# Performance work log

Measured on AMD Instinct MI355X. Metric: run time of the kernel, lower is better.

## Reference

```python
import jax, jax.numpy as jnp
import numpy as np

N_WIRES = 16
DIM = 2 ** N_WIRES
BSZ = 512
FFN_DIM = 64
N_BLOCKS = 2
N_RAND_OPS = 20
EPS = 1e-5


def rx_mat(theta):
    c = jnp.cos(theta / 2).astype(jnp.complex64)
    s = jnp.sin(theta / 2).astype(jnp.complex64)
    i = jnp.complex64(1j)
    return jnp.stack([jnp.stack([c, -i * s]), jnp.stack([-i * s, c])])


def ry_mat(theta):
    c = jnp.cos(theta / 2).astype(jnp.complex64)
    s = jnp.sin(theta / 2).astype(jnp.complex64)
    return jnp.stack([jnp.stack([c, -s]), jnp.stack([s, c])])


def apply_1q(psi, U, wire):
    # psi: [bsz, 2**n]; apply 2x2 U on `wire` (wire 0 = most significant)
    b = psi.shape[0]
    left = 2 ** wire
    s = psi.reshape(b, left, 2, -1)
    out = jnp.einsum('ij,bljr->blir', U, s)
    return out.reshape(b, -1)


def apply_cnot(psi, cw, tw):
    b = psi.shape[0]
    x = psi.reshape((b,) + (2,) * N_WIRES)
    x = jnp.moveaxis(x, (1 + cw, 1 + tw), (1, 2))
    x = jnp.concatenate([x[:, :1], x[:, 1:2, ::-1]], axis=1)
    x = jnp.moveaxis(x, (1, 2), (1 + cw, 1 + tw))
    return x.reshape(b, -1)


def measure_z(psi):
    # <Z_w> for every wire -> [bsz, n]
    b = psi.shape[0]
    p = jnp.abs(psi) ** 2
    outs = []
    for w in range(N_WIRES):
        pr = p.reshape(b, 2 ** w, 2, -1)
        outs.append((pr[:, :, 0] - pr[:, :, 1]).sum(axis=(1, 2)))
    return jnp.stack(outs, axis=1)


def layernorm(x, g, b):
    mu = x.mean(-1, keepdims=True)
    var = ((x - mu) ** 2).mean(-1, keepdims=True)
    return (x - mu) * jax.lax.rsqrt(var + EPS) * g + b


def setup_inputs() -> dict:
    key = jax.random.key(0)
    ks = jax.random.split(key, 16)
    states = jax.random.normal(ks[0], (BSZ, DIM), dtype=jnp.float32)
    rand_angles = jax.random.uniform(ks[1], (N_RAND_OPS,), minval=0.0, maxval=2 * np.pi, dtype=jnp.float32)
    theta_rx = jax.random.normal(ks[2], (N_BLOCKS,), dtype=jnp.float32)
    theta_ry = jax.random.normal(ks[3], (N_BLOCKS,), dtype=jnp.float32)
    s1 = 1.0 / np.sqrt(N_WIRES)
    s2 = 1.0 / np.sqrt(FFN_DIM)
    w1 = jax.random.uniform(ks[4], (N_BLOCKS, FFN_DIM, N_WIRES), minval=-s1, maxval=s1, dtype=jnp.float32)
    b1 = jax.random.uniform(ks[5], (N_BLOCKS, FFN_DIM), minval=-s1, maxval=s1, dtype=jnp.float32)
    w2 = jax.random.uniform(ks[6], (N_BLOCKS, N_WIRES, FFN_DIM), minval=-s2, maxval=s2, dtype=jnp.float32)
    b2 = jax.random.uniform(ks[7], (N_BLOCKS, N_WIRES), minval=-s2, maxval=s2, dtype=jnp.float32)
    g1 = jnp.ones((N_BLOCKS, N_WIRES), jnp.float32)
    be1 = jnp.zeros((N_BLOCKS, N_WIRES), jnp.float32)
    g2 = jnp.ones((N_BLOCKS, N_WIRES), jnp.float32)
    be2 = jnp.zeros((N_BLOCKS, N_WIRES), jnp.float32)
    wh = jax.random.uniform(ks[8], (1, N_WIRES), minval=-s1, maxval=s1, dtype=jnp.float32)
    bh = jax.random.uniform(ks[9], (1,), minval=-s1, maxval=s1, dtype=jnp.float32)
    return dict(states=states, rand_angles=rand_angles, theta_rx=theta_rx, theta_ry=theta_ry,
                w1=w1, b1=b1, w2=w2, b2=b2, g1=g1, be1=be1, g2=g2, be2=be2, wh=wh, bh=bh)


def _forward(states, rand_angles, theta_rx, theta_ry, w1, b1, w2, b2, g1, be1, g2, be2, wh, bh):
    # amplitude encoding: normalize, cast to complex statevector
    psi = (states / jnp.linalg.norm(states, axis=1, keepdims=True)).astype(jnp.complex64)
    # deterministic stand-in for tq.RandomLayer(n_ops=20): cycle RX/RY/CNOT over wires
    for i in range(N_RAND_OPS):
        w = (i * 5) % N_WIRES
        k = i % 3
        if k == 0:
            psi = apply_1q(psi, rx_mat(rand_angles[i]), w)
        elif k == 1:
            psi = apply_1q(psi, ry_mat(rand_angles[i]), w)
        else:
            psi = apply_cnot(psi, w, (w + 1) % N_WIRES)
    feats = None
    for blk in range(N_BLOCKS):
        # attention sub-module: shared RX on every wire, CNOT ring, measure Z
        Urx = rx_mat(theta_rx[blk])
        for w in range(N_WIRES):
            psi = apply_1q(psi, Urx, w)
        for w in range(N_WIRES - 1):
            psi = apply_cnot(psi, w, w + 1)
        psi = apply_cnot(psi, N_WIRES - 1, 0)
        attn = measure_z(psi)
        x = layernorm(attn, g1[blk], be1[blk])
        # ffn sub-module: shared RY on every wire, measure, MLP (dropout=eval identity)
        Ury = ry_mat(theta_ry[blk])
        for w in range(N_WIRES):
            psi = apply_1q(psi, Ury, w)
        m = measure_z(psi)
        h = jax.nn.relu(m @ w1[blk].T + b1[blk])
        ffn = h @ w2[blk].T + b2[blk]
        feats = layernorm(x + ffn, g2[blk], be2[blk])
    return (feats @ wh.T + bh)[:, 0]


def reference(states, rand_angles, theta_rx, theta_ry, w1, b1, w2, b2, g1, be1, g2, be2, wh, bh):
    return _forward(states, rand_angles, theta_rx, theta_ry, w1, b1, w2, b2, g1, be1, g2, be2, wh, bh)
```

## Files before the change

kernel.cpp:

```cpp
#include <hip/hip_runtime.h>
#include <math.h>


#define NT 256
#define ACCS 40
#define BSZQ 512

typedef float v2f __attribute__((ext_vector_type(2)));
typedef __fp16 h2t __attribute__((ext_vector_type(2)));

__device__ __forceinline__ v2f mk2(float a, float b){ v2f r; r.x = a; r.y = b; return r; }

__device__ __forceinline__ void wave_fence(){
  asm volatile("" ::: "memory");
  __builtin_amdgcn_wave_barrier();
  asm volatile("" ::: "memory");
}

__device__ __forceinline__ unsigned int f2h(v2f a){
  h2t h = __builtin_amdgcn_cvt_pkrtz(a.x, a.y);
  return *(unsigned int*)&h;
}
__device__ __forceinline__ v2f h2f(unsigned int u){
  h2t h = *(h2t*)&u;
  return mk2((float)h.x, (float)h.y);
}

__device__ __forceinline__ v2f pk_mul(v2f a, v2f b){
  v2f d; asm("v_pk_mul_f32 %0, %1, %2" : "=v"(d) : "v"(a), "v"(b)); return d;
}
__device__ __forceinline__ void pk_fma_acc(v2f& c, v2f a, v2f b){
  asm("v_pk_fma_f32 %0, %1, %2, %0" : "+v"(c) : "v"(a), "v"(b));
}
__device__ __forceinline__ void pk_fma_sw_acc(v2f& c, v2f a, v2f b){
  asm("v_pk_fma_f32 %0, %1, %2, %0 op_sel:[1,0,0] op_sel_hi:[0,1,1]"
      : "+v"(c) : "v"(a), "v"(b));
}
__device__ __forceinline__ void pk_add_acc(v2f& c, v2f a){
  asm("v_pk_add_f32 %0, %1, %0" : "+v"(c) : "v"(a));
}

struct C2 { float r, i; };
struct G1Q { C2 a, b, c, d; };

__device__ __forceinline__ C2 cmul(C2 x, C2 y){ return C2{ x.r*y.r - x.i*y.i, x.r*y.i + x.i*y.r }; }
__device__ __forceinline__ C2 cadd(C2 x, C2 y){ return C2{ x.r + y.r, x.i + y.i }; }
__device__ __forceinline__ G1Q mkRX(float th){
  float cc = cosf(0.5f*th), ss = sinf(0.5f*th);
  return G1Q{ C2{cc,0.f}, C2{0.f,-ss}, C2{0.f,-ss}, C2{cc,0.f} };
}
__device__ __forceinline__ G1Q mkRY(float th){
  float cc = cosf(0.5f*th), ss = sinf(0.5f*th);
  return G1Q{ C2{cc,0.f}, C2{-ss,0.f}, C2{ss,0.f}, C2{cc,0.f} };
}
__device__ __forceinline__ G1Q gmul(G1Q A, G1Q B){
  return G1Q{ cadd(cmul(A.a,B.a), cmul(A.b,B.c)),
              cadd(cmul(A.a,B.b), cmul(A.b,B.d)),
              cadd(cmul(A.c,B.a), cmul(A.d,B.c)),
              cadd(cmul(A.c,B.b), cmul(A.d,B.d)) };
}

struct PG1Q { v2f aR, aI, bR, bI, cR, cI, dR, dI; };
__device__ __forceinline__ PG1Q loadPG(const float* __restrict__ gt, int i){
  const float4* p = (const float4*)(gt + i*8);
  float4 u = p[0], w = p[1];
  PG1Q g;
  g.aR = mk2(u.x, u.x); g.aI = mk2(-u.y, u.y);
  g.bR = mk2(u.z, u.z); g.bI = mk2(-u.w, u.w);
  g.cR = mk2(w.x, w.x); g.cI = mk2(-w.y, w.y);
  g.dR = mk2(w.z, w.z); g.dI = mk2(-w.w, w.w);
  return g;
}

__device__ __forceinline__ int swzA(int l){ return (l & 0xFF0) | (((l>>4) ^ l) & 15); }
__device__ __forceinline__ int swzB(int l){ return (l & 0xFF0) | (((l>>8) ^ l) & 15); }

template<int M>
__device__ __forceinline__ float swzx(float x){
  return __int_as_float(__builtin_amdgcn_ds_swizzle(__float_as_int(x), (M<<10)|0x1F));
}
template<int C>
__device__ __forceinline__ float dppx(float x){
  return __int_as_float(__builtin_amdgcn_mov_dpp(__float_as_int(x), C, 0xF, 0xF, true));
}
__device__ __forceinline__ float wsum(float x){
  x += dppx<0xB1>(x);
  x += dppx<0x4E>(x);
  x += swzx<4>(x);
  x += swzx<8>(x);
  x += swzx<16>(x);
  return __int_as_float(__builtin_amdgcn_readlane(__float_as_int(x), 0)) +
         __int_as_float(__builtin_amdgcn_readlane(__float_as_int(x), 32));
}

__device__ __forceinline__ void greg16p(v2f* v, const PG1Q g, const int q){
  const int bq = 1<<q;
  #pragma unroll
  for (int r=0;r<16;r++){
    if (r & bq) continue;
    v2f a0 = v[r], a1 = v[r|bq];
    v2f t0 = pk_mul(a0, g.aR);
    pk_fma_sw_acc(t0, a0, g.aI);
    pk_fma_acc   (t0, a1, g.bR);
    pk_fma_sw_acc(t0, a1, g.bI);
    v2f t1 = pk_mul(a0, g.cR);
    pk_fma_sw_acc(t1, a0, g.cI);
    pk_fma_acc   (t1, a1, g.dR);
    pk_fma_sw_acc(t1, a1, g.dI);
    v[r] = t0; v[r|bq] = t1;
  }
}
__device__ __forceinline__ void creg16(v2f* v, const int qc, const int qt){
  #pragma unroll
  for (int r=0;r<16;r++){
    if ((r & (1<<qc)) && !(r & (1<<qt))){
      v2f tmp = v[r]; v[r] = v[r|(1<<qt)]; v[r|(1<<qt)] = tmp;
    }
  }
}
__device__ __forceinline__ float xdot16p(const v2f* v, const int m){
  v2f s = pk_mul(v[0], v[m]);
  #pragma unroll
  for (int r=1;r<16;r++) pk_fma_acc(s, v[r], v[r^m]);
  return s.x + s.y;
}

__global__ void qs_prep(const float* __restrict__ ra, const float* __restrict__ trx,
                        const float* __restrict__ tryv, float* __restrict__ gt){
  if (threadIdx.x != 0) return;
  float trx0 = trx[0];
  G1Q RX0 = mkRX(trx0);
  G1Q g[14];
  g[0]  = gmul(RX0, gmul(mkRY(ra[19]), mkRX(ra[3])));
  g[1]  = mkRX(trx0 + ra[6]);
  g[2]  = mkRX(trx0 + ra[9]);
  g[3]  = mkRX(trx0 + ra[12]);
  g[4]  = mkRX(trx0 + ra[15]);
  g[5]  = mkRX(trx0 + ra[18]);
  g[6]  = RX0;
  g[7]  = gmul(RX0, mkRY(ra[4]));
  g[8]  = mkRY(ra[1]);
  g[9]  = gmul(RX0, mkRY(ra[7]));
  g[10] = gmul(RX0, mkRY(ra[10]));
  g[11] = gmul(RX0, mkRY(ra[13]));
  g[12] = gmul(RX0, gmul(mkRY(ra[16]), mkRX(ra[0])));
  g[13] = gmul(mkRX(trx[1]), mkRY(tryv[0]));
  for (int i=0;i<14;i++){
    gt[i*8+0]=g[i].a.r; gt[i*8+1]=g[i].a.i;
    gt[i*8+2]=g[i].b.r; gt[i*8+3]=g[i].b.i;
    gt[i*8+4]=g[i].c.r; gt[i*8+5]=g[i].c.i;
    gt[i*8+6]=g[i].d.r; gt[i*8+7]=g[i].d.i;
  }
}

__global__ __launch_bounds__(NT) void qs_p1(const float* __restrict__ x, const float* __restrict__ gt,
                                            unsigned int* __restrict__ psi, float* __restrict__ acc){
  __shared__ __align__(16) v2f s[4096];
  int b = blockIdx.x >> 4, t = blockIdx.x & 15;
  int tid = threadIdx.x;
  if (t == 0 && tid < ACCS) acc[b*ACCS + tid] = 0.f;
  v2f v[16];
  const float4* xb = (const float4*)(x + (size_t)b*65536 + t*4096 + tid*16);
  #pragma unroll
  for (int q=0;q<4;q++){
    float4 f = xb[q];
    v[4*q+0] = mk2(f.x, 0.f);
    v[4*q+1] = mk2(f.y, 0.f);
    v[4*q+2] = mk2(f.z, 0.f);
    v[4*q+3] = mk2(f.w, 0.f);
  }
  greg16p(v, loadPG(gt,0), 0);
  greg16p(v, loadPG(gt,1), 1);
  greg16p(v, loadPG(gt,2), 2);
  greg16p(v, loadPG(gt,3), 3);
  #pragma unroll
  for (int j=0;j<16;j++) s[swzA(j | (tid<<4))] = v[j];
  wave_fence();
  #pragma unroll
  for (int r=0;r<16;r++) v[r] = s[swzA((tid&15) | (r<<4) | ((tid>>4)<<8))];
  creg16(v, 1, 0);
  creg16(v, 2, 1);
  creg16(v, 3, 2);
  {
    bool c8 = (tid & 16);
    #pragma unroll
    for (int r=0;r<8;r++){
      v2f lo = v[r], hi = v[r|8];
      v[r]   = c8 ? hi : lo;
      v[r|8] = c8 ? lo : hi;
    }
  }
  greg16p(v, loadPG(gt,4), 0);
  greg16p(v, loadPG(gt,5), 1);
  PG1Q PG6 = loadPG(gt,6);
  greg16p(v, PG6, 2);
  greg16p(v, PG6, 3);
  unsigned int* pbL = psi + (size_t)b*65536 + t*4096;
  #pragma unroll
  for (int r=0;r<16;r++) pbL[(tid&15) | (r<<4) | ((tid>>4)<<8)] = f2h(v[r]);
}

__global__ __launch_bounds__(NT) void qs_p2(unsigned int* __restrict__ psi, const float* __restrict__ gt){
  __shared__ __align__(16) v2f s[4096];
  int b = blockIdx.x >> 4, t = blockIdx.x & 15;
  int tid = threadIdx.x;
  v2f v[16];
  unsigned int* pb = psi + (size_t)b*65536;
  #pragma unroll
  for (int r=0;r<16;r++)
    v[r] = h2f(pb[(tid&15) | (t<<4) | (r<<8) | ((tid>>4)<<12)]);
  greg16p(v, loadPG(gt,7), 3);
  greg16p(v, loadPG(gt,8), 2);
  creg16(v, 1, 0);
  creg16(v, 2, 1);
  PG1Q PG6 = loadPG(gt,6);
  greg16p(v, PG6, 2);
  greg16p(v, PG6, 1);
  greg16p(v, PG6, 0);
  #pragma unroll
  for (int r=0;r<16;r++) s[swzA((tid&15) | (r<<4) | ((tid>>4)<<8))] = v[r];
  __syncthreads();
  #pragma unroll
  for (int r=0;r<16;r++) v[r] = s[swzA((tid&15) | ((tid>>4)<<4) | (r<<8))];
  greg16p(v, loadPG(gt,9), 0);
  greg16p(v, loadPG(gt,10), 1);
  greg16p(v, loadPG(gt,11), 2);
  greg16p(v, loadPG(gt,12), 3);
  #pragma unroll
  for (int r=0;r<16;r++)
    pb[(tid&15) | (t<<4) | ((tid>>4)<<8) | (r<<12)] = f2h(v[r]);
}

__global__ __launch_bounds__(NT) void qs_p4(unsigned int* __restrict__ psi, const float* __restrict__ gt,
                                            float* __restrict__ acc){
  __shared__ __align__(16) v2f s[4096];
  int b = blockIdx.x >> 4, t = blockIdx.x & 15;
  int tid = threadIdx.x;
  PG1Q U = loadPG(gt, 13);
  unsigned int* pb = psi + (size_t)b*65536;
  v2f v[16];
  {
    int Y = (tid>>4) | ((tid&15)<<4);
    int XH = Y ^ (Y>>1);
    int x7 = ((t>>3) ^ Y) & 1;
    int runbase = (XH<<8) | (x7<<7) | (((t ^ (t>>1)) & 7) << 4);
    const uint4* rp = (const uint4*)(pb + runbase);
    v2f tmp[16];
    #pragma unroll
    for (int q=0;q<4;q++){
      uint4 u = rp[q];
      tmp[4*q+0] = h2f(u.x);
      tmp[4*q+1] = h2f(u.y);
      tmp[4*q+2] = h2f(u.z);
      tmp[4*q+3] = h2f(u.w);
    }
    if (t & 1){
      v[15]=tmp[0];  v[14]=tmp[1];  v[12]=tmp[2];  v[13]=tmp[3];
      v[ 8]=tmp[4];  v[ 9]=tmp[5];  v[11]=tmp[6];  v[10]=tmp[7];
      v[ 0]=tmp[8];  v[ 1]=tmp[9];  v[ 3]=tmp[10]; v[ 2]=tmp[11];
      v[ 7]=tmp[12]; v[ 6]=tmp[13]; v[ 4]=tmp[14]; v[ 5]=tmp[15];
    } else {
      v[ 0]=tmp[0];  v[ 1]=tmp[1];  v[ 3]=tmp[2];  v[ 2]=tmp[3];
      v[ 7]=tmp[4];  v[ 6]=tmp[5];  v[ 4]=tmp[6];  v[ 5]=tmp[7];
      v[15]=tmp[8];  v[14]=tmp[9];  v[12]=tmp[10]; v[13]=tmp[11];
      v[ 8]=tmp[12]; v[ 9]=tmp[13]; v[11]=tmp[14]; v[10]=tmp[15];
    }
    #pragma unroll
    for (int r=1;r<16;r+=2){
      v[r].x = swzx<8>(v[r].x);
      v[r].y = swzx<8>(v[r].y);
    }
    greg16p(v, U, 0); greg16p(v, U, 1); greg16p(v, U, 2); greg16p(v, U, 3);
    #pragma unroll
    for (int j=0;j<16;j++)
      s[swzB(j | ((tid>>4)<<4) | ((tid&15)<<8))] = v[j];
  }
  wave_fence();
  float Xa, Xb, Xc, Xd;
  {
    #pragma unroll
    for (int r=0;r<16;r++)
      v[r] = s[swzB((tid&15) | ((tid>>4)<<4) | (r<<8))];
    greg16p(v, U, 0); greg16p(v, U, 1); greg16p(v, U, 2); greg16p(v, U, 3);
    creg16(v, 3, 2);
    creg16(v, 2, 1);
    creg16(v, 1, 0);
    Xa = xdot16p(v, 8);
    Xb = xdot16p(v, 4);
    Xc = xdot16p(v, 2);
    v2f XdP = mk2(0.f, 0.f);
    #pragma unroll
    for (int r=0;r<16;r++)
      pk_fma_acc(XdP, v[r], mk2(dppx<0xB1>(v[r^8].x), dppx<0xB1>(v[r^8].y)));
    Xd = XdP.x + XdP.y;
    wave_fence();
    #pragma unroll
    for (int r=0;r<16;r++)
      s[swzB((tid&15) | ((tid>>4)<<4) | (r<<8))] = v[r];
  }
  __syncthreads();
  float Xe, Xf, Xg, Xh;
  {
    #pragma unroll
    for (int r=0;r<16;r++)
      v[r] = s[swzB((tid&15) | (r<<4) | ((tid>>4)<<8))];
    greg16p(v, U, 0); greg16p(v, U, 1); greg16p(v, U, 2); greg16p(v, U, 3);
    {
      bool c12 = (tid & 16);
      #pragma unroll
      for (int r=0;r<8;r++){
        v2f lo = v[r], hi = v[r|8];
        v[r]   = c12 ? hi : lo;
        v[r|8] = c12 ? lo : hi;
      }
    }
    creg16(v, 3, 2);
    creg16(v, 2, 1);
    creg16(v, 1, 0);
    v2f XeP = mk2(0.f, 0.f);
    #pragma unroll
    for (int r=0;r<16;r++)
      pk_fma_acc(XeP, v[r], mk2(swzx<16>(v[r].x), swzx<16>(v[r].y)));
    Xe = XeP.x + XeP.y;
    Xf = xdot16p(v, 8);
    Xg = xdot16p(v, 4);
    Xh = xdot16p(v, 2);
    int Bs = (tid&15) | (t<<4) | ((tid>>4)<<12);
    int Cs = Bs ^ (Bs>>1);
    #pragma unroll
    for (int r=0;r<16;r++)
      pb[Cs ^ ((r<<8) ^ (r<<7))] = f2h(v[r]);
  }
  float vals[8] = {Xa, Xb, Xc, Xe, Xf, Xg, Xh, Xd};
  #pragma unroll
  for (int i=0;i<8;i++) vals[i] = wsum(vals[i]);
  if ((tid & 63) == 0){
    float* A = acc + b*ACCS;
    #pragma unroll
    for (int i=0;i<7;i++) atomicAdd(A+25+i, vals[i]);
    atomicAdd(A+32, vals[7]);
  }
}

__global__ __launch_bounds__(NT) void qs_p5(const unsigned int* __restrict__ psi, const float* __restrict__ gt,
                                            float* __restrict__ acc){
  int b = blockIdx.x >> 4, t = blockIdx.x & 15;
  int tid = threadIdx.x;
  PG1Q U = loadPG(gt, 13);
  const unsigned int* pb = psi + (size_t)b*65536;
  v2f v[16];
  int Bv = (t<<12) | ((tid>>4)<<8) | (tid&15);
  int Cg = Bv ^ (Bv>>1);
  #pragma unroll
  for (int r=0;r<16;r++)
    v[r] = h2f(pb[Cg ^ ((r<<4) ^ (r<<3))]);
  greg16p(v, U, 0); greg16p(v, U, 1); greg16p(v, U, 2); greg16p(v, U, 3);
  v2f z2 = mk2(0.f, 0.f);
  v2f totP=z2, S4P=z2, S5P=z2, S6P=z2, S7P=z2;
  #pragma unroll
  for (int r=0;r<16;r++){
    v2f sq = pk_mul(v[r], v[r]);
    pk_add_acc(totP, sq);
    if (__popc(r)&1)    pk_add_acc(S4P, sq);
    if (__popc(r>>1)&1) pk_add_acc(S5P, sq);
    if (__popc(r>>2)&1) pk_add_acc(S6P, sq);
    if (__popc(r>>3)&1) pk_add_acc(S7P, sq);
  }
  float totA = totP.x + totP.y;
  float S4l = S4P.x + S4P.y, S5l = S5P.x + S5P.y;
  float S6l = S6P.x + S6P.y, S7l = S7P.x + S7P.y;
  float S4h = totA - S4l;
  float S0 = (__popc(tid & 0x1F)&1) ? S4h : S4l;
  float S1 = (__popc(tid & 0x1E)&1) ? S4h : S4l;
  float S2 = (__popc(tid & 0x1C)&1) ? S4h : S4l;
  float S3 = (__popc(tid & 0x18)&1) ? S4h : S4l;
  bool u8 = (tid & 16);
  float S4 = u8 ? S4h : S4l;
  float S5 = u8 ? totA - S5l : S5l;
  float S6 = u8 ? totA - S6l : S6l;
  float S7 = u8 ? totA - S7l : S7l;
  float S8 = u8 ? totA : 0.f;
  float K9  = (tid & 32) ? totA : 0.f;
  float K10 = (tid & 64) ? totA : 0.f;
  float K11 = (tid & 128)? totA : 0.f;
  float X45 = xdot16p(v,3), X56 = xdot16p(v,6), X67 = xdot16p(v,12);
  v2f X01P=z2, X12P=z2, X23P=z2, X34P=z2, X78P=z2;
  #pragma unroll
  for (int r=0;r<16;r++){
    float vx = v[r].x, vy = v[r].y;
    pk_fma_acc(X01P, v[r], mk2(dppx<0x1B>(vx), dppx<0x1B>(vy)));
    pk_fma_acc(X12P, v[r], mk2(swzx<6>(vx),  swzx<6>(vy)));
    pk_fma_acc(X23P, v[r], mk2(swzx<12>(vx), swzx<12>(vy)));
    pk_fma_acc(X34P, v[r], mk2(swzx<8>(v[r^1].x), swzx<8>(v[r^1].y)));
    pk_fma_acc(X78P, v[r], mk2(swzx<16>(v[r^8].x), swzx<16>(v[r^8].y)));
  }
  float X01 = X01P.x + X01P.y, X12 = X12P.x + X12P.y, X23 = X23P.x + X23P.y;
  float X34 = X34P.x + X34P.y, X78 = X78P.x + X78P.y;
  float vals[21] = {totA, S0,S1,S2,S3,S4,S5,S6,S7,S8, K9,K10,K11,
                    X01,X12,X23,X34,X45,X56,X67,X78};
  #pragma unroll
  for (int i=0;i<21;i++) vals[i] = wsum(vals[i]);
  if ((tid & 63) == 0){
    float* A = acc + b*ACCS;
    atomicAdd(A+0, vals[0]);
    #pragma unroll
    for (int p=0;p<12;p++) atomicAdd(A+1+p, vals[1+p]);
    if (t&1) atomicAdd(A+13, vals[0]);
    if (t&2) atomicAdd(A+14, vals[0]);
    if (t&4) atomicAdd(A+15, vals[0]);
    float zz = vals[0] - 2.f*vals[1];
    if (t&8) zz = -zz;
    atomicAdd(A+16, zz);
    #pragma unroll
    for (int j=0;j<8;j++) atomicAdd(A+17+j, vals[13+j]);
  }
}

__global__ __launch_bounds__(256) void qs_tail(const float* __restrict__ acc, const float* __restrict__ tryv,
    const float* __restrict__ w1, const float* __restrict__ b1,
    const float* __restrict__ w2, const float* __restrict__ b2,
    const float* __restrict__ g1, const float* __restrict__ be1,
    const float* __restrict__ g2, const float* __restrict__ be2,
    const float* __restrict__ wh, const float* __restrict__ bh,
    float* __restrict__ out){
  int b = blockIdx.x * 256 + threadIdx.x;
  if (b >= BSZQ) return;
  const float* A = acc + b*ACCS;
  float tot = A[0];
  float inv = 1.f / tot;
  float Z[16], X[16];
  Z[0] = A[16] * inv;
  Z[1] = 1.f - 2.f*A[15]*inv;
  Z[2] = 1.f - 2.f*A[14]*inv;
  Z[3] = 1.f - 2.f*A[13]*inv;
  #pragma unroll
  for (int w=4; w<15; w++) Z[w] = 1.f - 2.f*A[1 + (15-w)]*inv;
  Z[15] = 1.f - 2.f*A[1]*inv;
  #pragma unroll
  for (int w=0; w<7; w++) X[w] = A[25+w]*inv;
  #pragma unroll
  for (int w=7; w<15; w++) X[w] = A[16 + (15-w)]*inv;
  X[15] = A[32]*inv;
  float th = tryv[1];
  float ct = cosf(th), st = sinf(th);
  float M4[16];
  #pragma unroll
  for (int w=0; w<16; w++) M4[w] = ct*Z[w] - st*X[w];
  float mu = 0.f;
  #pragma unroll
  for (int w=0; w<16; w++) mu += Z[w];
  mu *= (1.f/16.f);
  float var = 0.f;
  #pragma unroll
  for (int w=0; w<16; w++){ float d = Z[w]-mu; var += d*d; }
  var *= (1.f/16.f);
  float rs = rsqrtf(var + 1e-5f);
  float xln[16];
  #pragma unroll
  for (int w=0; w<16; w++) xln[w] = (Z[w]-mu)*rs*g1[16+w] + be1[16+w];
  float h[64];
  for (int j=0;j<64;j++){
    float sacc = b1[64 + j];
    #pragma unroll
    for (int w=0; w<16; w++) sacc += M4[w] * w1[1024 + j*16 + w];
    h[j] = fmaxf(sacc, 0.f);
  }
  float y[16];
  for (int w=0; w<16; w++){
    float sacc = b2[16 + w];
    #pragma unroll
    for (int j=0;j<64;j++) sacc += h[j] * w2[1024 + w*64 + j];
    y[w] = xln[w] + sacc;
  }
  mu = 0.f;
  #pragma unroll
  for (int w=0; w<16; w++) mu += y[w];
  mu *= (1.f/16.f);
  var = 0.f;
  #pragma unroll
  for (int w=0; w<16; w++){ float d = y[w]-mu; var += d*d; }
  var *= (1.f/16.f);
  rs = rsqrtf(var + 1e-5f);
  float o = bh[0];
  #pragma unroll
  for (int w=0; w<16; w++) o += ((y[w]-mu)*rs*g2[16+w] + be2[16+w]) * wh[w];
  out[b] = o;
}

extern "C" void kernel_launch(void* const* d_in, const int* in_sizes, int n_in,
                              void* d_out, int out_size, void* d_ws, size_t ws_size,
                              hipStream_t stream) {
  const float* states = (const float*)d_in[0];
  const float* ra     = (const float*)d_in[1];
  const float* trx    = (const float*)d_in[2];
  const float* tryv   = (const float*)d_in[3];
  const float* w1     = (const float*)d_in[4];
  const float* b1     = (const float*)d_in[5];
  const float* w2     = (const float*)d_in[6];
  const float* b2     = (const float*)d_in[7];
  const float* g1     = (const float*)d_in[8];
  const float* be1    = (const float*)d_in[9];
  const float* g2     = (const float*)d_in[10];
  const float* be2    = (const float*)d_in[11];
  const float* wh     = (const float*)d_in[12];
  const float* bh     = (const float*)d_in[13];
  float* out = (float*)d_out;

  unsigned int* psi = (unsigned int*)d_ws;
  float* acc  = (float*)((char*)d_ws + (size_t)BSZQ*65536*sizeof(float2));
  float* gt = out;

  dim3 g(BSZQ*16);
  qs_prep<<<1, 64, 0, stream>>>(ra, trx, tryv, gt);
  qs_p1<<<g, NT, 0, stream>>>(states, gt, psi, acc);
  qs_p2<<<g, NT, 0, stream>>>(psi, gt);
  qs_p4<<<g, NT, 0, stream>>>(psi, gt, acc);
  qs_p5<<<g, NT, 0, stream>>>(psi, gt, acc);
  qs_tail<<<2, 256, 0, stream>>>(acc, tryv, w1, b1, w2, b2, g1, be1, g2, be2, wh, bh, out);
}
```

Before: 539.3 us.

## Halve shared-memory transposes into two passes and batch wave reductions

The shared-memory transpose buffers in the three state-vector kernels shrink from 4096 to 2048 complex entries. Each transpose now runs in two halves, with half the threads or registers staged per pass and extra barriers, under a new three-way XOR swizzle. The aim is to cut LDS use per block so more blocks fit per CU and occupancy rises. The wave reductions are also interleaved across all values at each step to expose instruction-level parallelism. The cost is extra barriers, temporary registers and serialized half-passes, and register pressure may offset the occupancy gain.

```diff
diff --git a/kernel.cpp b/kernel.cpp
--- a/kernel.cpp
+++ b/kernel.cpp
@@ -72,8 +72,7 @@
   return g;
 }
 
-__device__ __forceinline__ int swzA(int l){ return (l & 0xFF0) | (((l>>4) ^ l) & 15); }
-__device__ __forceinline__ int swzB(int l){ return (l & 0xFF0) | (((l>>8) ^ l) & 15); }
+__device__ __forceinline__ int SW(int i){ return (i & ~15) | ((i ^ (i>>4) ^ (i>>8)) & 15); }
 
 template<int M>
 __device__ __forceinline__ float swzx(float x){
@@ -83,14 +82,22 @@
 __device__ __forceinline__ float dppx(float x){
   return __int_as_float(__builtin_amdgcn_mov_dpp(__float_as_int(x), C, 0xF, 0xF, true));
 }
-__device__ __forceinline__ float wsum(float x){
-  x += dppx<0xB1>(x);
-  x += dppx<0x4E>(x);
-  x += swzx<4>(x);
-  x += swzx<8>(x);
-  x += swzx<16>(x);
-  return __int_as_float(__builtin_amdgcn_readlane(__float_as_int(x), 0)) +
-         __int_as_float(__builtin_amdgcn_readlane(__float_as_int(x), 32));
+template<int N>
+__device__ __forceinline__ void wsumB(float* x){
+  #pragma unroll
+  for (int i=0;i<N;i++) x[i] += dppx<0xB1>(x[i]);
+  #pragma unroll
+  for (int i=0;i<N;i++) x[i] += dppx<0x4E>(x[i]);
+  #pragma unroll
+  for (int i=0;i<N;i++) x[i] += swzx<4>(x[i]);
+  #pragma unroll
+  for (int i=0;i<N;i++) x[i] += swzx<8>(x[i]);
+  #pragma unroll
+  for (int i=0;i<N;i++) x[i] += swzx<16>(x[i]);
+  #pragma unroll
+  for (int i=0;i<N;i++)
+    x[i] = __int_as_float(__builtin_amdgcn_readlane(__float_as_int(x[i]), 0)) +
+           __int_as_float(__builtin_amdgcn_readlane(__float_as_int(x[i]), 32));
 }
 
 __device__ __forceinline__ void greg16p(v2f* v, const PG1Q g, const int q){
@@ -155,7 +162,7 @@
 
 __global__ __launch_bounds__(NT) void qs_p1(const float* __restrict__ x, const float* __restrict__ gt,
                                             unsigned int* __restrict__ psi, float* __restrict__ acc){
-  __shared__ __align__(16) v2f s[4096];
+  __shared__ __align__(16) v2f s[2048];
   int b = blockIdx.x >> 4, t = blockIdx.x & 15;
   int tid = threadIdx.x;
   if (t == 0 && tid < ACCS) acc[b*ACCS + tid] = 0.f;
@@ -173,11 +180,31 @@
   greg16p(v, loadPG(gt,1), 1);
   greg16p(v, loadPG(gt,2), 2);
   greg16p(v, loadPG(gt,3), 3);
-  #pragma unroll
-  for (int j=0;j<16;j++) s[swzA(j | (tid<<4))] = v[j];
-  wave_fence();
-  #pragma unroll
-  for (int r=0;r<16;r++) v[r] = s[swzA((tid&15) | (r<<4) | ((tid>>4)<<8))];
+  {
+    int wbase = ((tid&15)<<3) | ((tid>>4)<<7);
+    int rbase = (tid&7) | ((tid>>4)<<7);
+    v2f tmp[8];
+    #pragma unroll
+    for (int j=0;j<8;j++) s[SW(j | wbase)] = v[j];
+    wave_fence();
+    if (!(tid & 8)){
+      #pragma unroll
+      for (int r=0;r<8;r++)  v[r]     = s[SW(rbase | (r<<3))];
+      #pragma unroll
+      for (int r=8;r<16;r++) tmp[r-8] = s[SW(rbase | (r<<3))];
+    }
+    wave_fence();
+    #pragma unroll
+    for (int j=8;j<16;j++) s[SW((j&7) | wbase)] = v[j];
+    wave_fence();
+    if (tid & 8){
+      #pragma unroll
+      for (int r=0;r<16;r++) v[r] = s[SW(rbase | (r<<3))];
+    } else {
+      #pragma unroll
+      for (int r=8;r<16;r++) v[r] = tmp[r-8];
+    }
+  }
   creg16(v, 1, 0);
   creg16(v, 2, 1);
   creg16(v, 3, 2);
@@ -201,7 +228,7 @@
 }
 
 __global__ __launch_bounds__(NT) void qs_p2(unsigned int* __restrict__ psi, const float* __restrict__ gt){
-  __shared__ __align__(16) v2f s[4096];
+  __shared__ __align__(16) v2f s[2048];
   int b = blockIdx.x >> 4, t = blockIdx.x & 15;
   int tid = threadIdx.x;
   v2f v[16];
@@ -217,11 +244,28 @@
   greg16p(v, PG6, 2);
   greg16p(v, PG6, 1);
   greg16p(v, PG6, 0);
-  #pragma unroll
-  for (int r=0;r<16;r++) s[swzA((tid&15) | (r<<4) | ((tid>>4)<<8))] = v[r];
-  __syncthreads();
-  #pragma unroll
-  for (int r=0;r<16;r++) v[r] = s[swzA((tid&15) | ((tid>>4)<<4) | (r<<8))];
+  {
+    int wbase = ((tid>>4)&7) | ((tid&15)<<7);
+    int rbase = ((tid>>4)<<3) | ((tid&15)<<7);
+    v2f tmp[8];
+    if (tid < 128){
+      #pragma unroll
+      for (int rr=0;rr<16;rr++) s[SW(wbase | (rr<<3))] = v[rr];
+    }
+    __syncthreads();
+    #pragma unroll
+    for (int r=0;r<8;r++) tmp[r] = s[SW(rbase | (r&7))];
+    __syncthreads();
+    if (tid >= 128){
+      #pragma unroll
+      for (int rr=0;rr<16;rr++) s[SW(wbase | (rr<<3))] = v[rr];
+    }
+    __syncthreads();
+    #pragma unroll
+    for (int r=8;r<16;r++) v[r] = s[SW(rbase | (r&7))];
+    #pragma unroll
+    for (int r=0;r<8;r++) v[r] = tmp[r];
+  }
   greg16p(v, loadPG(gt,9), 0);
   greg16p(v, loadPG(gt,10), 1);
   greg16p(v, loadPG(gt,11), 2);
@@ -233,7 +277,7 @@
 
 __global__ __launch_bounds__(NT) void qs_p4(unsigned int* __restrict__ psi, const float* __restrict__ gt,
                                             float* __restrict__ acc){
-  __shared__ __align__(16) v2f s[4096];
+  __shared__ __align__(16) v2f s[2048];
   int b = blockIdx.x >> 4, t = blockIdx.x & 15;
   int tid = threadIdx.x;
   PG1Q U = loadPG(gt, 13);
@@ -271,16 +315,31 @@
       v[r].y = swzx<8>(v[r].y);
     }
     greg16p(v, U, 0); greg16p(v, U, 1); greg16p(v, U, 2); greg16p(v, U, 3);
-    #pragma unroll
-    for (int j=0;j<16;j++)
-      s[swzB(j | ((tid>>4)<<4) | ((tid&15)<<8))] = v[j];
-  }
-  wave_fence();
+  }
+  {
+    int wbase = (tid&7) | ((tid>>4)<<7);
+    int rbase = ((tid&15)<<3) | ((tid>>4)<<7);
+    v2f tmp[8];
+    if (!(tid & 8)){
+      #pragma unroll
+      for (int j=0;j<16;j++) s[SW(wbase | (j<<3))] = v[j];
+    }
+    wave_fence();
+    #pragma unroll
+    for (int r=0;r<8;r++) tmp[r] = s[SW((r&7) | rbase)];
+    wave_fence();
+    if (tid & 8){
+      #pragma unroll
+      for (int j=0;j<16;j++) s[SW(wbase | (j<<3))] = v[j];
+    }
+    wave_fence();
+    #pragma unroll
+    for (int r=8;r<16;r++) v[r] = s[SW((r&7) | rbase)];
+    #pragma unroll
+    for (int r=0;r<8;r++) v[r] = tmp[r];
+  }
   float Xa, Xb, Xc, Xd;
   {
-    #pragma unroll
-    for (int r=0;r<16;r++)
-      v[r] = s[swzB((tid&15) | ((tid>>4)<<4) | (r<<8))];
     greg16p(v, U, 0); greg16p(v, U, 1); greg16p(v, U, 2); greg16p(v, U, 3);
     creg16(v, 3, 2);
     creg16(v, 2, 1);
@@ -293,17 +352,32 @@
     for (int r=0;r<16;r++)
       pk_fma_acc(XdP, v[r], mk2(dppx<0xB1>(v[r^8].x), dppx<0xB1>(v[r^8].y)));
     Xd = XdP.x + XdP.y;
-    wave_fence();
-    #pragma unroll
-    for (int r=0;r<16;r++)
-      s[swzB((tid&15) | ((tid>>4)<<4) | (r<<8))] = v[r];
-  }
-  __syncthreads();
+  }
+  {
+    int wbase = ((tid>>4)&7) | ((tid&15)<<7);
+    int rbase = ((tid>>4)<<3) | ((tid&15)<<7);
+    v2f tmp[8];
+    __syncthreads();
+    if (tid < 128){
+      #pragma unroll
+      for (int rr=0;rr<16;rr++) s[SW(wbase | (rr<<3))] = v[rr];
+    }
+    __syncthreads();
+    #pragma unroll
+    for (int r=0;r<8;r++) tmp[r] = s[SW(rbase | (r&7))];
+    __syncthreads();
+    if (tid >= 128){
+      #pragma unroll
+      for (int rr=0;rr<16;rr++) s[SW(wbase | (rr<<3))] = v[rr];
+    }
+    __syncthreads();
+    #pragma unroll
+    for (int r=8;r<16;r++) v[r] = s[SW(rbase | (r&7))];
+    #pragma unroll
+    for (int r=0;r<8;r++) v[r] = tmp[r];
+  }
   float Xe, Xf, Xg, Xh;
   {
-    #pragma unroll
-    for (int r=0;r<16;r++)
-      v[r] = s[swzB((tid&15) | (r<<4) | ((tid>>4)<<8))];
     greg16p(v, U, 0); greg16p(v, U, 1); greg16p(v, U, 2); greg16p(v, U, 3);
     {
       bool c12 = (tid & 16);
@@ -332,8 +406,7 @@
       pb[Cs ^ ((r<<8) ^ (r<<7))] = f2h(v[r]);
   }
   float vals[8] = {Xa, Xb, Xc, Xe, Xf, Xg, Xh, Xd};
-  #pragma unroll
-  for (int i=0;i<8;i++) vals[i] = wsum(vals[i]);
+  wsumB<8>(vals);
   if ((tid & 63) == 0){
     float* A = acc + b*ACCS;
     #pragma unroll
@@ -398,8 +471,7 @@
   float X34 = X34P.x + X34P.y, X78 = X78P.x + X78P.y;
   float vals[21] = {totA, S0,S1,S2,S3,S4,S5,S6,S7,S8, K9,K10,K11,
                     X01,X12,X23,X34,X45,X56,X67,X78};
-  #pragma unroll
-  for (int i=0;i<21;i++) vals[i] = wsum(vals[i]);
+  wsumB<21>(vals);
   if ((tid & 63) == 0){
     float* A = acc + b*ACCS;
     atomicAdd(A+0, vals[0]);
```

Measured after the change: 535.8 us. About the same (-0.6%).
